# Optimization experiments

Measured on AMD Instinct MI355X. Metric: run time of the kernel, lower is better.

Reference implementation:

```python
import jax, jax.numpy as jnp
import numpy as np

TAU = 1.1      # LIF membrane time constant
ALPHA = 4.0    # sigmoid surrogate sharpness (spikingjelly default)
EPS = 1e-5     # BatchNorm eps
SCALE = 0.125  # attention scale


def lif(x, v_th):
    # Single-step LIF, v init 0, decay_input=True: v = x / tau; spike = H(v - v_th)
    # Straight-through: forward heaviside, backward sigmoid surrogate derivative.
    u = x / TAU - v_th
    sg = jax.nn.sigmoid(ALPHA * u)
    return sg + jax.lax.stop_gradient((u >= 0.0).astype(x.dtype) - sg)


def bn(x, gamma, beta):
    # BatchNorm1d in training mode on [B, C, N]: stats over (B, N) per channel
    mean = jnp.mean(x, axis=(0, 2), keepdims=True)
    var = jnp.var(x, axis=(0, 2), keepdims=True)
    return gamma[None, :, None] * (x - mean) * jax.lax.rsqrt(var + EPS) + beta[None, :, None]


def conv1x1(w, x):
    # Conv1d kernel_size=1: pointwise channel mix, x: [B,C,N], w: [O,C]
    return jnp.einsum('oc,bcn->bon', w, x)


def setup_inputs() -> dict:
    key = jax.random.key(0)
    B, C, N = 32, 512, 1024
    ks = jax.random.split(key, 6)
    s = 1.0 / np.sqrt(C)
    inp = {"x": jax.random.normal(ks[0], (B, C, N), jnp.float32)}
    for name, k in zip(["q", "k", "v", "proj"], ks[1:5]):
        inp[name + "_w"] = jax.random.uniform(k, (C, C), jnp.float32, -s, s)
        inp[name + "_gamma"] = jnp.ones((C,), jnp.float32)
        inp[name + "_beta"] = jnp.zeros((C,), jnp.float32)
    inp["proj_b"] = jax.random.uniform(ks[5], (C,), jnp.float32, -s, s)
    return inp


def reference(x, q_w, q_gamma, q_beta, k_w, k_gamma, k_beta, v_w, v_gamma, v_beta,
              proj_w, proj_b, proj_gamma, proj_beta):
    # x: [B, C, N]
    q = lif(bn(conv1x1(q_w, x), q_gamma, q_beta), 1.0)  # [B,C,N] spikes
    k = lif(bn(conv1x1(k_w, x), k_gamma, k_beta), 1.0)
    v = lif(bn(conv1x1(v_w, x), v_gamma, v_beta), 1.0)
    # linear (softmax-free) attention: kv[c,d] = sum_n k[n,c] v[n,d]
    kv = jnp.einsum('bcn,bdn->bcd', k, v)               # [B,C,C]
    attn = jnp.einsum('bcn,bcd->bdn', q, kv) * SCALE    # [B,C,N] (already transposed back)
    attn = lif(attn, 0.5)
    out = conv1x1(proj_w, attn) + proj_b[None, :, None]
    return lif(bn(out, proj_gamma, proj_beta), 1.0)
```

## Files before the change

### kernel.cpp

```cpp
#include <hip/hip_runtime.h>
#include <cstddef>


#define CC 512
#define BB 32
#define NN 1024

typedef __attribute__((ext_vector_type(4))) float v4f;
typedef unsigned char uchar;
typedef unsigned long long ull;

__device__ __forceinline__ ushort f2bf(float f) {
  unsigned u = __float_as_uint(f);
  unsigned r = (u + 0x7FFFu + ((u >> 16) & 1u)) >> 16;
  return (ushort)r;
}

__device__ __forceinline__ uchar f2e4(float v) {
  if (v < 0.5f) return 0;
  unsigned u = __float_as_uint(v);
  unsigned r = u + 0x7FFFFu + ((u >> 20) & 1u);
  int e8 = (int)((r >> 23) & 0xFF) - 120;
  unsigned m = (r >> 20) & 7u;
  unsigned byte = ((unsigned)e8 << 3) | m;
  return (uchar)(byte > 0x7Eu ? 0x7Eu : byte);
}

__device__ __forceinline__ uchar f2e4s(float v) {
  const uchar s = (v < 0.f) ? 0x80 : 0x00;
  float a = fabsf(v);
  if (a >= 464.f) return s | 0x7E;
  if (a < 0.015625f) {
    int q = (int)rintf(a * 512.f);
    return s | (uchar)q;
  }
  const int e = (int)((__float_as_uint(a) >> 23) & 0xFF) - 126;
  const float scale = __uint_as_float((unsigned)(4 - e + 127) << 23);
  const int q = (int)rintf(a * scale);
  int code = ((e - 1 + 7) << 3) + (q - 8);
  if (code > 0x7E) code = 0x7E;
  return s | (uchar)code;
}

__device__ __forceinline__ void gload16(const void* g, void* l) {
  __builtin_amdgcn_global_load_lds(
      (const __attribute__((address_space(1))) unsigned int*)g,
      (__attribute__((address_space(3))) unsigned int*)l, 16, 0, 0);
}

template <int EPI>
__global__ __launch_bounds__(256) void gemm8(const uchar* __restrict__ A,
                                             const uchar* __restrict__ B,
                                             void* __restrict__ Cout,
                                             const float* __restrict__ bias,
                                             int M, int N, int K,
                                             long sA, long sB, long sC) {
  __shared__ __align__(16) uchar lds[32768];
  const int b = blockIdx.z;
  const uchar* Ab = A + (size_t)b * sA;
  const uchar* Bb = B + (size_t)b * sB;
  const int m0 = blockIdx.y * 128, n0 = blockIdx.x * 128;
  const int tid = threadIdx.x;
  const int wave = tid >> 6, lane = tid & 63;
  const int lrow = lane & 15, lquad = lane >> 4;
  const int wr = wave >> 1, wc = wave & 1;
  const int laneoff = 16 * lrow + 256 * (lane >> 5) + 8 * (lquad & 1);

  v4f acc[4][4];
#pragma unroll
  for (int i = 0; i < 4; i++)
#pragma unroll
    for (int j = 0; j < 4; j++) acc[i][j] = (v4f)0.f;

  const uchar* gA0 = Ab + (size_t)(m0 + 32 * wave + lrow) * K + lquad * 16;
  const uchar* gA1 = gA0 + (size_t)16 * K;
  const uchar* gB0 = Bb + (size_t)(n0 + 32 * wave + lrow) * K + lquad * 16;
  const uchar* gB1 = gB0 + (size_t)16 * K;
  uchar* lA00 = lds + (2 * wave) * 1024;
  uchar* lA01 = lds + (8 + 2 * wave) * 1024;
  uchar* lA10 = lA00 + 1024;
  uchar* lA11 = lA01 + 1024;
  uchar* lB00 = lds + 16384 + (2 * wave) * 1024;
  uchar* lB01 = lds + 16384 + (8 + 2 * wave) * 1024;
  uchar* lB10 = lB00 + 1024;
  uchar* lB11 = lB01 + 1024;

  for (int k0 = 0; k0 < K; k0 += 128) {
    gload16(gA0, lA00);
    gload16(gA0 + 64, lA01);
    gload16(gA1, lA10);
    gload16(gA1 + 64, lA11);
    gload16(gB0, lB00);
    gload16(gB0 + 64, lB01);
    gload16(gB1, lB10);
    gload16(gB1 + 64, lB11);
    gA0 += 128; gA1 += 128; gB0 += 128; gB1 += 128;
    __syncthreads();
#pragma unroll
    for (int h = 0; h < 4; h++) {
      const uchar* ra = lds + (size_t)(((h >> 1) * 8 + 4 * wr) * 1024 + 512 * (h & 1)) + laneoff;
      const uchar* rb = lds + 16384 + (size_t)(((h >> 1) * 8 + 4 * wc) * 1024 + 512 * (h & 1)) + laneoff;
      long af[4], bf[4];
#pragma unroll
      for (int i = 0; i < 4; i++) af[i] = *(const long*)(ra + i * 1024);
#pragma unroll
      for (int j = 0; j < 4; j++) bf[j] = *(const long*)(rb + j * 1024);
#pragma unroll
      for (int i = 0; i < 4; i++)
#pragma unroll
        for (int j = 0; j < 4; j++)
          acc[i][j] = __builtin_amdgcn_mfma_f32_16x16x32_fp8_fp8(af[i], bf[j], acc[i][j], 0, 0, 0);
    }
    __syncthreads();
  }

  if (EPI == 3) {
#pragma unroll
    for (int mi = 0; mi < 4; mi++)
#pragma unroll
      for (int r = 0; r < 4; r++) {
        const float bi = bias[m0 + 64 * wr + 16 * mi + lquad * 4 + r];
#pragma unroll
        for (int ni = 0; ni < 4; ni++) acc[mi][ni][r] += bi;
      }
  }

#pragma unroll
  for (int mi = 0; mi < 4; mi++) {
    const int row0 = m0 + 64 * wr + 16 * mi + lquad * 4;
#pragma unroll
    for (int ni = 0; ni < 4; ni++) {
      const int col = n0 + 64 * wc + 16 * ni + lrow;
#pragma unroll
      for (int r = 0; r < 4; r++) {
        const float v = acc[mi][ni][r];
        if (EPI == 2 || EPI == 3) {
          ushort* cp = (ushort*)Cout + (size_t)b * sC + (size_t)(row0 + r) * N + col;
          *cp = f2bf(v);
        } else if (EPI == 0) {
          uchar* cp = (uchar*)Cout + (size_t)b * sC + (size_t)(row0 + r) * N + col;
          *cp = f2e4(v);
        } else {
          uchar* cp = (uchar*)Cout + (size_t)b * sC + (size_t)(row0 + r) * N + col;
          const float u = (v * 0.125f) / 1.1f - 0.5f;
          *cp = (u >= 0.f) ? (uchar)0x38 : (uchar)0;
        }
      }
    }
  }
}

__global__ __launch_bounds__(256) void stats_part_k(const ushort* __restrict__ in,
                                                    float* __restrict__ P,
                                                    long bstride) {
  const int part = blockIdx.x, c = blockIdx.y;
  const int tid = threadIdx.x;
  const int bi = part * 4 + (tid >> 6);
  const int lane = tid & 63;
  const ushort* p = in + (size_t)bi * bstride + (size_t)c * 1024 + lane * 16;
  float s = 0.f, s2 = 0.f;
  const uint4 u0 = *(const uint4*)p;
  const uint4 u1 = *(const uint4*)(p + 8);
  const unsigned w8[8] = {u0.x, u0.y, u0.z, u0.w, u1.x, u1.y, u1.z, u1.w};
#pragma unroll
  for (int t = 0; t < 8; t++) {
    float f0 = __uint_as_float(w8[t] << 16);
    float f1 = __uint_as_float(w8[t] & 0xFFFF0000u);
    s += f0 + f1;
    s2 += f0 * f0 + f1 * f1;
  }
#pragma unroll
  for (int off = 32; off > 0; off >>= 1) {
    s += __shfl_down(s, off, 64);
    s2 += __shfl_down(s2, off, 64);
  }
  __shared__ float rs[4], rq[4];
  const int w = tid >> 6;
  if (lane == 0) { rs[w] = s; rq[w] = s2; }
  __syncthreads();
  if (tid == 0) {
    float2 o = make_float2(rs[0] + rs[1] + rs[2] + rs[3],
                           rq[0] + rq[1] + rq[2] + rq[3]);
    *(float2*)(P + (size_t)(c * 8 + part) * 2) = o;
  }
}

__global__ __launch_bounds__(256) void finalize8_k(const float* __restrict__ P,
                                                   float2* __restrict__ F,
                                                   const float* __restrict__ g0, const float* __restrict__ b0,
                                                   const float* __restrict__ g1, const float* __restrict__ b1,
                                                   const float* __restrict__ g2, const float* __restrict__ b2,
                                                   int nch) {
  const int c = blockIdx.x * 256 + threadIdx.x;
  if (c >= nch) return;
  const float* pc = P + (size_t)c * 16;
  float S = 0.f, Q = 0.f;
#pragma unroll
  for (int t = 0; t < 8; t++) { S += pc[2 * t]; Q += pc[2 * t + 1]; }
  const float mean = S * (1.f / 32768.f);
  const float var = fmaxf(Q * (1.f / 32768.f) - mean * mean, 0.f);
  const float rinv = 1.f / sqrtf(var + 1e-5f);
  const int sec = c >> 9, cl = c & 511;
  const float g = (sec == 0 ? g0 : sec == 1 ? g1 : g2)[cl];
  const float bt = (sec == 0 ? b0 : sec == 1 ? b1 : b2)[cl];
  const float a = g * rinv;
  F[c] = make_float2(a, bt - mean * a);
}

__global__ __launch_bounds__(256) void apply_kv8(const ushort* __restrict__ qkv,
                                                 uchar* __restrict__ k8,
                                                 uchar* __restrict__ v8,
                                                 const float2* __restrict__ F) {
  const int sec = blockIdx.y;
  const size_t t = (size_t)blockIdx.x * 256 + threadIdx.x;
  const size_t i = t * 8;
  const int b = (int)(i >> 19);
  const int rem = (int)(i & 524287);
  const int c = rem >> 10, n = rem & 1023;
  const float2 ab = F[512 + 512 * sec + c];
  const ushort* src = qkv + (size_t)b * (1536 * 1024) + (size_t)(512 + 512 * sec + c) * 1024 + n;
  const uint4 u = *(const uint4*)src;
  const unsigned w4[4] = {u.x, u.y, u.z, u.w};
  ull packed = 0;
#pragma unroll
  for (int j = 0; j < 4; j++) {
    float f0 = __uint_as_float(w4[j] << 16);
    float f1 = __uint_as_float(w4[j] & 0xFFFF0000u);
    ull b0 = (ab.x * f0 + ab.y >= 1.1f) ? 0x38ull : 0ull;
    ull b1 = (ab.x * f1 + ab.y >= 1.1f) ? 0x38ull : 0ull;
    packed |= (b0 << (16 * j)) | (b1 << (16 * j + 8));
  }
  uchar* dst = (sec ? v8 : k8) + (size_t)b * (CC * NN) + (size_t)c * 1024 + n;
  *(ull*)dst = packed;
}

__global__ __launch_bounds__(256) void apply_qT8(const ushort* __restrict__ qkv,
                                                 uchar* __restrict__ q8,
                                                 const float2* __restrict__ F) {
  __shared__ uchar tile[32][33];
  const int b = blockIdx.z;
  const int n0 = blockIdx.x * 32, c0 = blockIdx.y * 32;
  const int tx = threadIdx.x & 31, ty = threadIdx.x >> 5;
  const ushort* in = qkv + (size_t)b * (1536 * 1024);
#pragma unroll
  for (int i = 0; i < 32; i += 8) {
    const int c = c0 + ty + i;
    const float2 ab = F[c];
    float f = __uint_as_float((unsigned)in[(size_t)c * 1024 + n0 + tx] << 16);
    tile[ty + i][tx] = (ab.x * f + ab.y >= 1.1f) ? (uchar)0x38 : (uchar)0;
  }
  __syncthreads();
  uchar* out = q8 + (size_t)b * (NN * CC);
  const int nl = threadIdx.x >> 3;
  const int cq = (threadIdx.x & 7) * 4;
  uchar4 v;
  v.x = tile[cq][nl]; v.y = tile[cq + 1][nl];
  v.z = tile[cq + 2][nl]; v.w = tile[cq + 3][nl];
  *(uchar4*)(out + (size_t)(n0 + nl) * CC + c0 + cq) = v;
}

__global__ __launch_bounds__(256) void apply_final_k(const ushort* __restrict__ in,
                                                     float* __restrict__ outp,
                                                     const float2* __restrict__ F) {
  const size_t idx = ((size_t)blockIdx.x * 256 + threadIdx.x) * 8;
  const int c = (int)((idx >> 10) & (CC - 1));
  const float2 ab = F[c];
  const uint4 u = *(const uint4*)(in + idx);
  const unsigned w4[4] = {u.x, u.y, u.z, u.w};
  float of[8];
#pragma unroll
  for (int i = 0; i < 4; i++) {
    float f0 = __uint_as_float(w4[i] << 16);
    float f1 = __uint_as_float(w4[i] & 0xFFFF0000u);
    of[2 * i]     = (ab.x * f0 + ab.y >= 1.1f) ? 1.f : 0.f;
    of[2 * i + 1] = (ab.x * f1 + ab.y >= 1.1f) ? 1.f : 0.f;
  }
  float* op = outp + idx;
  *(float4*)op = make_float4(of[0], of[1], of[2], of[3]);
  *(float4*)(op + 4) = make_float4(of[4], of[5], of[6], of[7]);
}

__global__ __launch_bounds__(256) void transpose_f32_8(const float* __restrict__ inp,
                                                       uchar* __restrict__ out) {
  __shared__ uchar tile[32][33];
  const int b = blockIdx.z;
  const int n0 = blockIdx.x * 32, c0 = blockIdx.y * 32;
  const int tx = threadIdx.x & 31, ty = threadIdx.x >> 5;
  const float* in = inp + (size_t)b * (CC * NN);
#pragma unroll
  for (int i = 0; i < 32; i += 8) {
    tile[ty + i][tx] = f2e4s(in[(size_t)(c0 + ty + i) * NN + n0 + tx]);
  }
  __syncthreads();
  uchar* o = out + (size_t)b * (NN * CC);
  const int nl = threadIdx.x >> 3;
  const int cq = (threadIdx.x & 7) * 4;
  uchar4 v;
  v.x = tile[cq][nl]; v.y = tile[cq + 1][nl];
  v.z = tile[cq + 2][nl]; v.w = tile[cq + 3][nl];
  *(uchar4*)(o + (size_t)(n0 + nl) * CC + c0 + cq) = v;
}

__global__ __launch_bounds__(256) void wcvt8_k(const float* __restrict__ w0, const float* __restrict__ w1,
                                               const float* __restrict__ w2, const float* __restrict__ w3,
                                               uchar* __restrict__ o0, uchar* __restrict__ o1,
                                               uchar* __restrict__ o2, uchar* __restrict__ o3) {
  const float* src;
  uchar* dst;
  switch (blockIdx.y) {
    case 0: src = w0; dst = o0; break;
    case 1: src = w1; dst = o1; break;
    case 2: src = w2; dst = o2; break;
    default: src = w3; dst = o3; break;
  }
  const int i = (blockIdx.x * 256 + threadIdx.x) * 4;
  float4 v = *(const float4*)(src + i);
  uchar4 o;
  o.x = f2e4s(v.x); o.y = f2e4s(v.y); o.z = f2e4s(v.z); o.w = f2e4s(v.w);
  *(uchar4*)(dst + i) = o;
}

extern "C" void kernel_launch(void* const* d_in, const int* in_sizes, int n_in,
                              void* d_out, int out_size, void* d_ws, size_t ws_size,
                              hipStream_t stream) {
  const float* x          = (const float*)d_in[0];
  const float* q_w        = (const float*)d_in[1];
  const float* q_gamma    = (const float*)d_in[2];
  const float* q_beta     = (const float*)d_in[3];
  const float* k_w        = (const float*)d_in[4];
  const float* k_gamma    = (const float*)d_in[5];
  const float* k_beta     = (const float*)d_in[6];
  const float* v_w        = (const float*)d_in[7];
  const float* v_gamma    = (const float*)d_in[8];
  const float* v_beta     = (const float*)d_in[9];
  const float* proj_w     = (const float*)d_in[10];
  const float* proj_gamma = (const float*)d_in[11];
  const float* proj_beta  = (const float*)d_in[12];
  const float* proj_b     = (const float*)d_in[13];

  char* base = (char*)d_ws;
  const size_t MB = 1u << 20;
  uchar*  xT8   = (uchar*)base;
  ushort* qkv   = (ushort*)(base + 16 * MB);
  uchar*  q8    = (uchar*)(base + 112 * MB);
  uchar*  k8    = (uchar*)(base + 128 * MB);
  uchar*  v8    = (uchar*)(base + 144 * MB);
  uchar*  kvT8  = (uchar*)(base + 160 * MB);
  uchar*  attnT8= (uchar*)(base + 168 * MB);
  uchar*  wqkv8 = (uchar*)(base + 184 * MB);
  uchar*  wp8   = wqkv8 + 3 * CC * CC;
  float*  P     = (float*)(base + 186 * MB);
  float*  Pp    = P + 1536 * 16;
  float2* F     = (float2*)(Pp + 512 * 16);
  ushort* outpre = qkv;
  float* dout = (float*)d_out;

  const long QKVL = (long)3 * CC * NN;
  const long TL   = (long)CC * NN;
  const long NCL  = (long)NN * CC;
  const long CNL  = (long)CC * NN;
  const long KVL  = (long)CC * CC;

  transpose_f32_8<<<dim3(NN / 32, CC / 32, BB), 256, 0, stream>>>(x, xT8);
  wcvt8_k<<<dim3(CC * CC / 1024, 4), 256, 0, stream>>>(
      q_w, k_w, v_w, proj_w, wqkv8, wqkv8 + CC * CC, wqkv8 + 2 * CC * CC, wp8);

  gemm8<2><<<dim3(NN / 128, 1536 / 128, BB), 256, 0, stream>>>(
      wqkv8, xT8, qkv, nullptr, 1536, NN, CC, 0, NCL, QKVL);

  stats_part_k<<<dim3(8, 1536), 256, 0, stream>>>(qkv, P, QKVL);
  finalize8_k<<<6, 256, 0, stream>>>(P, F, q_gamma, q_beta, k_gamma, k_beta,
                                     v_gamma, v_beta, 1536);

  apply_qT8<<<dim3(NN / 32, CC / 32, BB), 256, 0, stream>>>(qkv, q8, F);
  apply_kv8<<<dim3(8192, 2), 256, 0, stream>>>(qkv, k8, v8, F);

  gemm8<0><<<dim3(CC / 128, CC / 128, BB), 256, 0, stream>>>(
      v8, k8, kvT8, nullptr, CC, CC, NN, CNL, CNL, KVL);
  gemm8<1><<<dim3(CC / 128, NN / 128, BB), 256, 0, stream>>>(
      q8, kvT8, attnT8, nullptr, NN, CC, CC, NCL, KVL, NCL);
  gemm8<3><<<dim3(NN / 128, CC / 128, BB), 256, 0, stream>>>(
      wp8, attnT8, outpre, proj_b, CC, NN, CC, 0, NCL, TL);

  stats_part_k<<<dim3(8, CC), 256, 0, stream>>>(outpre, Pp, TL);
  finalize8_k<<<2, 256, 0, stream>>>(Pp, F, proj_gamma, proj_beta, proj_gamma,
                                     proj_beta, proj_gamma, proj_beta, CC);
  apply_final_k<<<8192, 256, 0, stream>>>(outpre, dout, F);
}
```

Measured before the change: 358.3 us.

## Permute fp8 K-dimension layout so GEMM reads 16-byte LDS fragments per lane

Producers of fp8 operands (weight conversion, transposes, k/v spike packing, GEMM epilogues writing fp8) now write the K dimension in a permuted order within each 64-element group. Each lane of the GEMM can then load one 16-byte vector from LDS holding two consecutive MFMA k-steps, replacing two 8-byte loads. The aim is to halve the LDS read instructions and simplify address math in the inner loop. The cost is a more complex index calculation in several producer kernels, and every consumer must agree on the permutation or results will be wrong.

Result: no change. 354.9 us (-0.9%).

```diff
diff --git a/kernel.cpp b/kernel.cpp
--- a/kernel.cpp
+++ b/kernel.cpp
@@ -7,6 +7,7 @@
 #define NN 1024
 
 typedef __attribute__((ext_vector_type(4))) float v4f;
+typedef __attribute__((ext_vector_type(2))) long v2l;
 typedef unsigned char uchar;
 typedef unsigned long long ull;
 
@@ -40,6 +41,13 @@
   int code = ((e - 1 + 7) << 3) + (q - 8);
   if (code > 0x7E) code = 0x7E;
   return s | (uchar)code;
+}
+
+__device__ __forceinline__ int perm64(int off) {
+  return ((off & 0x18) << 1) | ((off & 0x20) >> 2) | (off & 7);
+}
+__device__ __forceinline__ int perm16(int g4) {
+  return ((g4 & 0x6) << 1) | ((g4 & 0x8) >> 2) | (g4 & 1);
 }
 
 __device__ __forceinline__ void gload16(const void* g, void* l) {
@@ -64,7 +72,6 @@
   const int wave = tid >> 6, lane = tid & 63;
   const int lrow = lane & 15, lquad = lane >> 4;
   const int wr = wave >> 1, wc = wave & 1;
-  const int laneoff = 16 * lrow + 256 * (lane >> 5) + 8 * (lquad & 1);
 
   v4f acc[4][4];
 #pragma unroll
@@ -97,19 +104,22 @@
     gA0 += 128; gA1 += 128; gB0 += 128; gB1 += 128;
     __syncthreads();
 #pragma unroll
-    for (int h = 0; h < 4; h++) {
-      const uchar* ra = lds + (size_t)(((h >> 1) * 8 + 4 * wr) * 1024 + 512 * (h & 1)) + laneoff;
-      const uchar* rb = lds + 16384 + (size_t)(((h >> 1) * 8 + 4 * wc) * 1024 + 512 * (h & 1)) + laneoff;
-      long af[4], bf[4];
-#pragma unroll
-      for (int i = 0; i < 4; i++) af[i] = *(const long*)(ra + i * 1024);
-#pragma unroll
-      for (int j = 0; j < 4; j++) bf[j] = *(const long*)(rb + j * 1024);
-#pragma unroll
-      for (int i = 0; i < 4; i++)
-#pragma unroll
-        for (int j = 0; j < 4; j++)
-          acc[i][j] = __builtin_amdgcn_mfma_f32_16x16x32_fp8_fp8(af[i], bf[j], acc[i][j], 0, 0, 0);
+    for (int g = 0; g < 2; g++) {
+      const uchar* ra = lds + (size_t)(((g << 3) + 4 * wr) * 1024) + 16 * lane;
+      const uchar* rb = lds + 16384 + (size_t)(((g << 3) + 4 * wc) * 1024) + 16 * lane;
+      v2l a16[4], b16[4];
+#pragma unroll
+      for (int i = 0; i < 4; i++) a16[i] = *(const v2l*)(ra + i * 1024);
+#pragma unroll
+      for (int j = 0; j < 4; j++) b16[j] = *(const v2l*)(rb + j * 1024);
+#pragma unroll
+      for (int h = 0; h < 2; h++)
+#pragma unroll
+        for (int i = 0; i < 4; i++)
+#pragma unroll
+          for (int j = 0; j < 4; j++)
+            acc[i][j] = __builtin_amdgcn_mfma_f32_16x16x32_fp8_fp8(
+                a16[i][h], b16[j][h], acc[i][j], 0, 0, 0);
     }
     __syncthreads();
   }
@@ -130,7 +140,8 @@
     const int row0 = m0 + 64 * wr + 16 * mi + lquad * 4;
 #pragma unroll
     for (int ni = 0; ni < 4; ni++) {
-      const int col = n0 + 64 * wc + 16 * ni + lrow;
+      const int col_lin = n0 + 64 * wc + 16 * ni + lrow;
+      const int col = (EPI <= 1) ? ((col_lin & ~63) | perm64(col_lin & 63)) : col_lin;
 #pragma unroll
       for (int r = 0; r < 4; r++) {
         const float v = acc[mi][ni][r];
@@ -230,7 +241,10 @@
     ull b1 = (ab.x * f1 + ab.y >= 1.1f) ? 0x38ull : 0ull;
     packed |= (b0 << (16 * j)) | (b1 << (16 * j + 8));
   }
-  uchar* dst = (sec ? v8 : k8) + (size_t)b * (CC * NN) + (size_t)c * 1024 + n;
+  const int n8 = n >> 3;
+  const int ggl = ((n8 & 3) << 1) | ((n8 >> 2) & 1);
+  const int np = (n & ~63) | (ggl << 3);
+  uchar* dst = (sec ? v8 : k8) + (size_t)b * (CC * NN) + (size_t)c * 1024 + np;
   *(ull*)dst = packed;
 }
 
@@ -256,7 +270,10 @@
   uchar4 v;
   v.x = tile[cq][nl]; v.y = tile[cq + 1][nl];
   v.z = tile[cq + 2][nl]; v.w = tile[cq + 3][nl];
-  *(uchar4*)(out + (size_t)(n0 + nl) * CC + c0 + cq) = v;
+  const int ctgt = c0 + cq;
+  const int g4 = (ctgt >> 2) & 15;
+  const int cp = (ctgt & ~63) | (perm16(g4) << 2);
+  *(uchar4*)(out + (size_t)(n0 + nl) * CC + cp) = v;
 }
 
 __global__ __launch_bounds__(256) void apply_final_k(const ushort* __restrict__ in,
@@ -298,7 +315,10 @@
   uchar4 v;
   v.x = tile[cq][nl]; v.y = tile[cq + 1][nl];
   v.z = tile[cq + 2][nl]; v.w = tile[cq + 3][nl];
-  *(uchar4*)(o + (size_t)(n0 + nl) * CC + c0 + cq) = v;
+  const int ctgt = c0 + cq;
+  const int g4 = (ctgt >> 2) & 15;
+  const int cp = (ctgt & ~63) | (perm16(g4) << 2);
+  *(uchar4*)(o + (size_t)(n0 + nl) * CC + cp) = v;
 }
 
 __global__ __launch_bounds__(256) void wcvt8_k(const float* __restrict__ w0, const float* __restrict__ w1,
@@ -317,7 +337,9 @@
   float4 v = *(const float4*)(src + i);
   uchar4 o;
   o.x = f2e4s(v.x); o.y = f2e4s(v.y); o.z = f2e4s(v.z); o.w = f2e4s(v.w);
-  *(uchar4*)(dst + i) = o;
+  const int g4 = (i >> 2) & 15;
+  const int ip = (i & ~63) | (perm16(g4) << 2);
+  *(uchar4*)(dst + ip) = o;
 }
 
 extern "C" void kernel_launch(void* const* d_in, const int* in_sizes, int n_in,
```
